# Performance work log

Hardware: AMD Instinct MI355X
Metric: run time of the kernel (lower is better)

Reference implementation:

```python
import jax, jax.numpy as jnp
import numpy as np
from math import sqrt

B, L, D, NH = 1, 2048, 1024, 16
HD = D // NH
EPS = 1e-5
NEG = -1e9


def setup_inputs() -> dict:
    key = jax.random.key(0)
    ks = jax.random.split(key, 5)
    x = jax.random.normal(ks[0], (B, L, D), jnp.float32)
    # causal additive mask (added to raw QK^T scores before /sqrt(d))
    causal = jnp.tril(jnp.ones((L, L), bool))
    m = jnp.where(causal, 0.0, NEG).astype(jnp.float32)[None, None]  # (1,1,L,L)
    init = lambda k, s: (0.02 * jax.random.normal(k, s)).astype(jnp.float32)
    return dict(
        x=x, m=m,
        wx_w=init(ks[1], (3 * D, D)), wx_b=jnp.zeros((3 * D,), jnp.float32),
        wo_w=init(ks[2], (D, D)), wo_b=jnp.zeros((D,), jnp.float32),
        ffn1_w=init(ks[3], (4 * D, D)), ffn1_b=jnp.zeros((4 * D,), jnp.float32),
        ffn2_w=init(ks[4], (D, 4 * D)), ffn2_b=jnp.zeros((D,), jnp.float32),
        ln1_w=jnp.float32(1.0), ln1_b=jnp.float32(0.0),
        ln2_w=jnp.float32(1.0), ln2_b=jnp.float32(0.0),
    )


def layer_norm(x, w, b):
    # scalar gain/bias, biased variance via E[x^2] - E[x]^2 (as in source)
    mu = x.mean(-1, keepdims=True)
    mu2 = (x * x).mean(-1, keepdims=True)
    sigma = jnp.sqrt(mu2 - mu * mu + EPS)
    return w * (x - mu) / sigma + b


def gelu(x):
    return x * 0.5 * (1 + jax.scipy.special.erf(x / sqrt(2.0)))


def reference(x, m, wx_w, wx_b, wo_w, wo_b, ffn1_w, ffn1_b, ffn2_w, ffn2_b,
              ln1_w, ln1_b, ln2_w, ln2_b):
    b, l, d = x.shape
    qkv = layer_norm(x, ln1_w, ln1_b) @ wx_w.T + wx_b          # (b,l,3d)
    q, k, v = [t.reshape(b, l, NH, HD) for t in jnp.split(qkv, 3, axis=-1)]
    # mask added BEFORE scaling by 1/sqrt(d) -- faithful to source
    scores = (jnp.einsum('bind,bjnd->bnij', q, k) + m) / sqrt(d)  # (b,nh,l,l)
    A = jax.nn.softmax(scores, axis=-1)
    mha = jnp.einsum('bnij,bjnd->bind', A, v).reshape(b, l, d)
    x = x + mha @ wo_w.T + wo_b
    h = layer_norm(x, ln2_w, ln2_b)
    return x + gelu(h @ ffn1_w.T + ffn1_b) @ ffn2_w.T + ffn2_b
```

## Files before the change

kernel.cpp:

```cpp
#include <hip/hip_runtime.h>

typedef short bf16x8 __attribute__((ext_vector_type(8)));
typedef float f32x4 __attribute__((ext_vector_type(4)));
typedef unsigned short u16;

__device__ __forceinline__ u16 f2b(float f) {
  unsigned u = __builtin_bit_cast(unsigned, f);
  u += 0x7fffu + ((u >> 16) & 1u);
  return (u16)(u >> 16);
}
__device__ __forceinline__ float b2f(u16 h) {
  unsigned u = ((unsigned)h) << 16;
  return __builtin_bit_cast(float, u);
}

__device__ __forceinline__ void gload16(const void* g, void* l) {
  __builtin_amdgcn_global_load_lds(
      (const __attribute__((address_space(1))) unsigned*)g,
      (__attribute__((address_space(3))) unsigned*)l, 16, 0, 0);
}

__global__ __launch_bounds__(256) void prep_kernel(
    const float* __restrict__ s0, int n0, const float* __restrict__ s1, int n1,
    const float* __restrict__ s2, int n2, const float* __restrict__ s3, int n3,
    u16* __restrict__ d0, u16* __restrict__ d1, u16* __restrict__ d2, u16* __restrict__ d3,
    const float* __restrict__ x, u16* __restrict__ lnout,
    const float* __restrict__ wp, const float* __restrict__ bp) {
  __shared__ float red[8];
  if (blockIdx.x < 1024) {
    long long total = ((long long)n0 + n1 + n2 + n3) >> 2;
    long long stride = 1024LL * 256;
    for (long long i = (long long)blockIdx.x * 256 + threadIdx.x; i < total; i += stride) {
      long long e = i << 2;
      const float* sp; u16* dp; long long off;
      if (e < n0)                { sp = s0; dp = d0; off = e; }
      else if (e < n0 + n1)      { sp = s1; dp = d1; off = e - n0; }
      else if (e < n0 + n1 + n2) { sp = s2; dp = d2; off = e - n0 - n1; }
      else                       { sp = s3; dp = d3; off = e - n0 - n1 - n2; }
      float4 v = *(const float4*)(sp + off);
      ushort4 o;
      o.x = f2b(v.x); o.y = f2b(v.y); o.z = f2b(v.z); o.w = f2b(v.w);
      *(ushort4*)(dp + off) = o;
    }
    return;
  }
  int row = blockIdx.x - 1024;
  const float* xr = x + (size_t)row * 1024;
  float4 v = ((const float4*)xr)[threadIdx.x];
  float lsum = v.x + v.y + v.z + v.w;
  float lsq = v.x * v.x + v.y * v.y + v.z * v.z + v.w * v.w;
#pragma unroll
  for (int off = 32; off; off >>= 1) {
    lsum += __shfl_down(lsum, off);
    lsq += __shfl_down(lsq, off);
  }
  int wv_ = threadIdx.x >> 6, ln_ = threadIdx.x & 63;
  if (ln_ == 0) { red[wv_] = lsum; red[4 + wv_] = lsq; }
  __syncthreads();
  if (threadIdx.x == 0) {
    float ts = red[0] + red[1] + red[2] + red[3];
    float ts2 = red[4] + red[5] + red[6] + red[7];
    red[0] = ts; red[4] = ts2;
  }
  __syncthreads();
  float mu = red[0] * (1.0f / 1024.0f);
  float mu2 = red[4] * (1.0f / 1024.0f);
  float inv = 1.0f / sqrtf(mu2 - mu * mu + 1e-5f);
  float gw = *wp, gb = *bp;
  ushort4 o;
  o.x = f2b(gw * (v.x - mu) * inv + gb);
  o.y = f2b(gw * (v.y - mu) * inv + gb);
  o.z = f2b(gw * (v.z - mu) * inv + gb);
  o.w = f2b(gw * (v.w - mu) * inv + gb);
  ((ushort4*)lnout)[(size_t)row * 256 + threadIdx.x] = o;
}

__global__ __launch_bounds__(256) void reduce2(
    const float* __restrict__ p, const float* __restrict__ bias,
    const float* __restrict__ resid, float* __restrict__ out) {
  int i = blockIdx.x * 256 + threadIdx.x;
  float4 a = ((const float4*)p)[i];
  float4 b = ((const float4*)p)[i + 524288];
  float4 r = ((const float4*)resid)[i];
  float4 bb = ((const float4*)bias)[i & 255];
  float4 o;
  o.x = a.x + b.x + r.x + bb.x;
  o.y = a.y + b.y + r.y + bb.y;
  o.z = a.z + b.z + r.z + bb.z;
  o.w = a.w + b.w + r.w + bb.w;
  ((float4*)out)[i] = o;
}

__global__ __launch_bounds__(256) void reduce_ln(
    const float* __restrict__ p, const float* __restrict__ bias,
    const float* __restrict__ resid, float* __restrict__ x1out,
    u16* __restrict__ lnout,
    const float* __restrict__ wp, const float* __restrict__ bp) {
  int row = blockIdx.x;
  int i = row * 256 + threadIdx.x;
  float4 a = ((const float4*)p)[i];
  float4 b = ((const float4*)p)[i + 524288];
  float4 r = ((const float4*)resid)[i];
  float4 bb = ((const float4*)bias)[threadIdx.x];
  float4 v;
  v.x = a.x + b.x + r.x + bb.x;
  v.y = a.y + b.y + r.y + bb.y;
  v.z = a.z + b.z + r.z + bb.z;
  v.w = a.w + b.w + r.w + bb.w;
  ((float4*)x1out)[i] = v;
  float lsum = v.x + v.y + v.z + v.w;
  float lsq = v.x * v.x + v.y * v.y + v.z * v.z + v.w * v.w;
#pragma unroll
  for (int off = 32; off; off >>= 1) {
    lsum += __shfl_down(lsum, off);
    lsq += __shfl_down(lsq, off);
  }
  __shared__ float red[8];
  int wv_ = threadIdx.x >> 6, ln_ = threadIdx.x & 63;
  if (ln_ == 0) { red[wv_] = lsum; red[4 + wv_] = lsq; }
  __syncthreads();
  if (threadIdx.x == 0) {
    float ts = red[0] + red[1] + red[2] + red[3];
    float ts2 = red[4] + red[5] + red[6] + red[7];
    red[0] = ts; red[4] = ts2;
  }
  __syncthreads();
  float mu = red[0] * (1.0f / 1024.0f);
  float mu2 = red[4] * (1.0f / 1024.0f);
  float inv = 1.0f / sqrtf(mu2 - mu * mu + 1e-5f);
  float gw = *wp, gb = *bp;
  ushort4 o;
  o.x = f2b(gw * (v.x - mu) * inv + gb);
  o.y = f2b(gw * (v.y - mu) * inv + gb);
  o.z = f2b(gw * (v.z - mu) * inv + gb);
  o.w = f2b(gw * (v.w - mu) * inv + gb);
  ((ushort4*)lnout)[i] = o;
}

#define BN 128
#define BMT 64
#define BK 64

template <int EPI, bool SPLITX>
__global__ __launch_bounds__(256, 3) void gemm_bt(
    const u16* __restrict__ A, const u16* __restrict__ W,
    const float* __restrict__ bias, const float* __restrict__ resid,
    void* __restrict__ Cout, u16* __restrict__ vtout, int M, int N, int K) {
  constexpr int MR = BMT / 32;
  __shared__ __align__(16) u16 sA[2][BMT * BK];
  __shared__ __align__(16) u16 sB[2][BN * BK];
  const int tid = threadIdx.x;

  const int gx = gridDim.x, gy = gridDim.y;
  int bx, by;
  {
    int oxy = blockIdx.y * gx + blockIdx.x;
    int xcd = oxy & 7, pos = oxy >> 3;
    if (SPLITX) {
      int bxp = gx >> 3;
      bx = xcd * bxp + pos % bxp;
      by = pos / bxp;
    } else {
      int byp = gy >> 3;
      by = xcd * byp + pos % byp;
      bx = pos / byp;
    }
  }

  const int l = tid & 63;
  const int w = tid >> 6;
  const int wm = w >> 1, wn = w & 1;
  const int lr = l & 15, lg = l >> 4;

  f32x4 acc[MR][4] = {};

  const int r_st = tid >> 3;
  const int s_st = tid & 7;

  const u16* Abase = A + (size_t)(by * BMT) * K;
  const u16* Wbase = W + (size_t)(bx * BN) * K;
  const int NK = K / (BK * (int)gridDim.z);
  const int ktbase = (int)blockIdx.z * NK;

  auto stage = [&](int buf, int kt) {
    const int k0 = (ktbase + kt) * BK;
#pragma unroll
    for (int i = 0; i < BMT / 32; i++) {
      int r = i * 32 + r_st;
      int ss = s_st ^ (r & 7);
      gload16(Abase + (size_t)r * K + k0 + ss * 8, &sA[buf][(i * 256 + tid) * 8]);
    }
#pragma unroll
    for (int i = 0; i < 4; i++) {
      int r = i * 32 + r_st;
      int ss = s_st ^ (r & 7);
      gload16(Wbase + (size_t)r * K + k0 + ss * 8, &sB[buf][(i * 256 + tid) * 8]);
    }
  };

  auto compute = [&](int buf) {
#pragma unroll
    for (int kk = 0; kk < 2; kk++) {
      bf16x8 a[MR], b[4];
#pragma unroll
      for (int mr = 0; mr < MR; mr++) {
        int row = wm * (BMT / 2) + mr * 16 + lr;
        int ss = (kk * 4 + lg) ^ (row & 7);
        a[mr] = *(const bf16x8*)&sA[buf][row * 64 + ss * 8];
      }
#pragma unroll
      for (int nr = 0; nr < 4; nr++) {
        int row = wn * 64 + nr * 16 + lr;
        int ss = (kk * 4 + lg) ^ (row & 7);
        b[nr] = *(const bf16x8*)&sB[buf][row * 64 + ss * 8];
      }
#pragma unroll
      for (int mr = 0; mr < MR; mr++)
#pragma unroll
        for (int nr = 0; nr < 4; nr++)
          acc[mr][nr] = __builtin_amdgcn_mfma_f32_16x16x32_bf16(a[mr], b[nr], acc[mr][nr], 0, 0, 0);
    }
  };

  stage(0, 0);
  asm volatile("s_waitcnt vmcnt(0)" ::: "memory");
  __syncthreads();
  for (int kt = 0; kt < NK; kt++) {
    if (kt + 1 < NK) stage((kt + 1) & 1, kt + 1);
    compute(kt & 1);
    asm volatile("s_waitcnt vmcnt(0)" ::: "memory");
    __syncthreads();
  }

  const int crow0 = by * BMT + wm * (BMT / 2);
  const int ccol0 = bx * BN + wn * 64;

  if (EPI == 4) {
    float* P4 = (float*)Cout + (size_t)blockIdx.z * (size_t)M * N;
#pragma unroll
    for (int nr = 0; nr < 4; nr++) {
      int col = ccol0 + nr * 16 + lr;
#pragma unroll
      for (int mr = 0; mr < MR; mr++) {
        int rowb = crow0 + mr * 16 + lg * 4;
#pragma unroll
        for (int r = 0; r < 4; r++)
          P4[(size_t)(rowb + r) * N + col] = acc[mr][nr][r];
      }
    }
    return;
  }

  if (EPI == 3 && ccol0 >= 2048) {
    const int hd0 = ccol0 - 2048;
#pragma unroll
    for (int nr = 0; nr < 4; nr++) {
      int hd = hd0 + nr * 16 + lr;
      float bv = bias[ccol0 + nr * 16 + lr];
#pragma unroll
      for (int mr = 0; mr < MR; mr++) {
        int m0 = crow0 + mr * 16 + lg * 4;
        ushort4 o;
        o.x = f2b(acc[mr][nr][0] + bv);
        o.y = f2b(acc[mr][nr][1] + bv);
        o.z = f2b(acc[mr][nr][2] + bv);
        o.w = f2b(acc[mr][nr][3] + bv);
        *(ushort4*)&vtout[(size_t)hd * 2048 + m0] = o;
      }
    }
    return;
  }

#pragma unroll
  for (int nr = 0; nr < 4; nr++) {
    int col = ccol0 + nr * 16 + lr;
    float bv = bias[col];
#pragma unroll
    for (int mr = 0; mr < MR; mr++) {
      int rowb = crow0 + mr * 16 + lg * 4;
#pragma unroll
      for (int r = 0; r < 4; r++) {
        float v = acc[mr][nr][r] + bv;
        size_t off = (size_t)(rowb + r) * N + col;
        if (EPI == 2) {
          float u = 0.7978845608f * (v + 0.044715f * v * v * v);
          u = fminf(15.0f, fmaxf(-15.0f, u));
          float e = __expf(2.0f * u);
          float g = 0.5f * v * (1.0f + (e - 1.0f) / (e + 1.0f));
          ((u16*)Cout)[off] = f2b(g);
        } else {
          ((u16*)Cout)[off] = f2b(v);
        }
      }
    }
  }
}

__global__ __launch_bounds__(256) void attn_kernel(
    const u16* __restrict__ qkv, const u16* __restrict__ vt,
    float* __restrict__ O0, float* __restrict__ O1, float* __restrict__ O2v,
    float* __restrict__ l0p, float* __restrict__ l1p, float* __restrict__ l2p) {
  const int i = (int)blockIdx.x;
  int qb, sec, nsec;
  if (i < 24)      { qb = 31 - i / 3;        sec = i % 3;        nsec = 3; }
  else if (i < 48) { qb = 23 - (i - 24) / 2; sec = (i - 24) & 1; nsec = 2; }
  else             { qb = 59 - i;            sec = 0;            nsec = 1; }
  const int nt = qb + 1;
  const int t0 = (nt * sec) / nsec;
  const int t1 = (nt * (sec + 1)) / nsec;

  const int h = blockIdx.y;
  __shared__ __align__(16) u16 sK[2][64 * 64];
  __shared__ __align__(16) u16 sV[2][64 * 64];
  __shared__ __align__(16) u16 P[4][16 * 72];
  const int tid = threadIdx.x;
  const int l = tid & 63, w = tid >> 6;
  const int lr = l & 15, lg = l >> 4;
  const int qrow0 = qb * 64 + w * 16;
  const u16* kbase = qkv + 1024 + h * 64;
  const u16* vbase = vt + (size_t)(h * 64) * 2048;

  const int r_st = tid >> 3;
  const int s_st = tid & 7;

  auto stage = [&](int buf, int t) {
    const int j0 = t * 64;
#pragma unroll
    for (int i2 = 0; i2 < 2; i2++) {
      int r = i2 * 32 + r_st;
      int ss = s_st ^ (r & 7);
      gload16(kbase + (size_t)(j0 + r) * 3072 + ss * 8, &sK[buf][(i2 * 256 + tid) * 8]);
    }
#pragma unroll
    for (int i2 = 0; i2 < 2; i2++) {
      int r = i2 * 32 + r_st;
      int ss = s_st ^ (r & 7);
      gload16(vbase + (size_t)r * 2048 + j0 + ss * 8, &sV[buf][(i2 * 256 + tid) * 8]);
    }
  };

  bf16x8 aq[2];
#pragma unroll
  for (int kk = 0; kk < 2; kk++)
    aq[kk] = *(const bf16x8*)&qkv[(size_t)(qrow0 + lr) * 3072 + h * 64 + kk * 32 + lg * 8];

  f32x4 oa[4];
  float l_r[4] = {0.f, 0.f, 0.f, 0.f};
#pragma unroll
  for (int d = 0; d < 4; d++) oa[d] = f32x4{0.f, 0.f, 0.f, 0.f};

  auto compute = [&](int buf, int t, bool masked) {
    const int j0 = t * 64;
    f32x4 s[4] = {};
#pragma unroll
    for (int kk = 0; kk < 2; kk++) {
#pragma unroll
      for (int c = 0; c < 4; c++) {
        int row = c * 16 + lr;
        int ss = (kk * 4 + lg) ^ (row & 7);
        bf16x8 kf = *(const bf16x8*)&sK[buf][row * 64 + ss * 8];
        s[c] = __builtin_amdgcn_mfma_f32_16x16x32_bf16(aq[kk], kf, s[c], 0, 0, 0);
      }
    }

#pragma unroll
    for (int r = 0; r < 4; r++) {
      const int q = qrow0 + lg * 4 + r;
      float rs = 0.f;
#pragma unroll
      for (int c = 0; c < 4; c++) {
        float p = __expf(s[c][r] * 0.03125f);
        if (masked) {
          int j = j0 + c * 16 + lr;
          p = (j > q) ? 0.f : p;
        }
        u16 pb = f2b(p);
        P[w][(lg * 4 + r) * 72 + c * 16 + lr] = pb;
        rs += b2f(pb);
      }
      l_r[r] += rs;
    }

#pragma unroll
    for (int kk = 0; kk < 2; kk++) {
      bf16x8 pa = *(const bf16x8*)&P[w][lr * 72 + kk * 32 + lg * 8];
#pragma unroll
      for (int d = 0; d < 4; d++) {
        int row = d * 16 + lr;
        int ss = (kk * 4 + lg) ^ (row & 7);
        bf16x8 bv = *(const bf16x8*)&sV[buf][row * 64 + ss * 8];
        oa[d] = __builtin_amdgcn_mfma_f32_16x16x32_bf16(pa, bv, oa[d], 0, 0, 0);
      }
    }
  };

  const int ntile = t1 - t0;
  stage(0, t0);
  asm volatile("s_waitcnt vmcnt(0)" ::: "memory");
  __syncthreads();
  for (int ti = 0; ti < ntile; ti++) {
    const int t = t0 + ti;
    if (ti + 1 < ntile) stage((ti + 1) & 1, t + 1);
    compute(ti & 1, t, t == nt - 1);
    asm volatile("s_waitcnt vmcnt(0)" ::: "memory");
    __syncthreads();
  }

  float* Op = (sec == 0) ? O0 : (sec == 1) ? O1 : O2v;
  float* lp = (sec == 0) ? l0p : (sec == 1) ? l1p : l2p;
#pragma unroll
  for (int r = 0; r < 4; r++) {
#pragma unroll
    for (int off = 1; off < 16; off <<= 1) l_r[r] += __shfl_xor(l_r[r], off);
    int q = qrow0 + lg * 4 + r;
    if (lr == 0) lp[q * 16 + h] = l_r[r];
#pragma unroll
    for (int d = 0; d < 4; d++)
      Op[(size_t)q * 1024 + h * 64 + d * 16 + lr] = oa[d][r];
  }
}

__global__ __launch_bounds__(256) void attn_combine(
    const float* __restrict__ O0, const float* __restrict__ O1,
    const float* __restrict__ O2v,
    const float* __restrict__ l0p, const float* __restrict__ l1p,
    const float* __restrict__ l2p, u16* __restrict__ mhab) {
  const int row = blockIdx.x;
  const int t = threadIdx.x;
  const int h = t >> 4;
  float4 v = ((const float4*)(O0 + (size_t)row * 1024))[t];
  float ls = l0p[row * 16 + h];
  if (row >= 768) {
    float4 v1 = ((const float4*)(O1 + (size_t)row * 1024))[t];
    v.x += v1.x; v.y += v1.y; v.z += v1.z; v.w += v1.w;
    ls += l1p[row * 16 + h];
  }
  if (row >= 1536) {
    float4 v2 = ((const float4*)(O2v + (size_t)row * 1024))[t];
    v.x += v2.x; v.y += v2.y; v.z += v2.z; v.w += v2.w;
    ls += l2p[row * 16 + h];
  }
  float inv = 1.0f / ls;
  ushort4 o;
  o.x = f2b(v.x * inv); o.y = f2b(v.y * inv);
  o.z = f2b(v.z * inv); o.w = f2b(v.w * inv);
  ((ushort4*)(mhab + (size_t)row * 1024))[t] = o;
}

extern "C" void kernel_launch(void* const* d_in, const int* in_sizes, int n_in,
                              void* d_out, int out_size, void* d_ws, size_t ws_size,
                              hipStream_t stream) {
  const float* x    = (const float*)d_in[0];
  const float* wx_w = (const float*)d_in[2];
  const float* wx_b = (const float*)d_in[3];
  const float* wo_w = (const float*)d_in[4];
  const float* wo_b = (const float*)d_in[5];
  const float* f1_w = (const float*)d_in[6];
  const float* f1_b = (const float*)d_in[7];
  const float* f2_w = (const float*)d_in[8];
  const float* f2_b = (const float*)d_in[9];
  const float* ln1w = (const float*)d_in[10];
  const float* ln1b = (const float*)d_in[11];
  const float* ln2w = (const float*)d_in[12];
  const float* ln2b = (const float*)d_in[13];

  char* ws = (char*)d_ws;
  u16*   ln_x  = (u16*)(ws + 0);
  float* l0p   = (float*)(ws + 0);
  float* l1p   = (float*)(ws + 131072);
  float* l2p   = (float*)(ws + 262144);
  u16*   qkv   = (u16*)(ws + 4194304);
  float* part  = (float*)(ws + 0);
  u16*   mhab  = (u16*)(ws + 16777216);
  float* x1    = (float*)(ws + 20971520);
  float* O0    = (float*)(ws + 20971520);
  u16*   hbuf  = (u16*)(ws + 29360128);
  u16*   vt    = (u16*)(ws + 33554432);
  u16*   f1o   = (u16*)(ws + 33554432);
  float* O1    = (float*)(ws + 37748736);
  float* O2v   = (float*)(ws + 46137344) - (size_t)1536 * 1024;
  u16*   wxb16 = (u16*)(ws + 50331648);
  u16*   wob16 = (u16*)(ws + 56623104);
  u16*   f1b16 = (u16*)(ws + 58720256);
  u16*   f2b16 = (u16*)(ws + 67108864);

  prep_kernel<<<3072, 256, 0, stream>>>(wx_w, 3145728, wo_w, 1048576, f1_w, 4194304, f2_w, 4194304,
                                        wxb16, wob16, f1b16, f2b16, x, ln_x, ln1w, ln1b);
  gemm_bt<3, true><<<dim3(24, 32), 256, 0, stream>>>(ln_x, wxb16, wx_b, nullptr, qkv, vt, 2048, 3072, 1024);
  attn_kernel<<<dim3(60, 16), 256, 0, stream>>>(qkv, vt, O0, O1, O2v, l0p, l1p, l2p);
  attn_combine<<<2048, 256, 0, stream>>>(O0, O1, O2v, l0p, l1p, l2p, mhab);
  gemm_bt<4, false><<<dim3(8, 32, 2), 256, 0, stream>>>(mhab, wob16, wo_b, nullptr, part, nullptr, 2048, 1024, 1024);
  reduce_ln<<<2048, 256, 0, stream>>>(part, wo_b, x, x1, hbuf, ln2w, ln2b);
  gemm_bt<2, true><<<dim3(32, 32), 256, 0, stream>>>(hbuf, f1b16, f1_b, nullptr, f1o, nullptr, 2048, 4096, 1024);
  gemm_bt<4, false><<<dim3(8, 32, 2), 256, 0, stream>>>(f1o, f2b16, f2_b, nullptr, part, nullptr, 2048, 1024, 4096);
  reduce2<<<2048, 256, 0, stream>>>(part, f2_b, x1, (float*)d_out);
}
```

Before: 157.2 us.

## Overlap remaining weight bf16 conversion with the QKV GEMM via extra blocks

The prep kernel now converts only the QKV projection weights to bf16. Conversion of the output-projection and FFN weights moves into extra blocks appended to the QKV GEMM grid (24 -> 32 columns), so it runs alongside the GEMM tiles instead of ahead of them. The GEMM gains a logical grid width parameter so tile swizzling ignores the extra blocks. This shortens the critical path before the first GEMM, at the cost of the conversion blocks competing with GEMM tiles for bandwidth and CU slots.

```diff
diff --git a/kernel.cpp b/kernel.cpp
--- a/kernel.cpp
+++ b/kernel.cpp
@@ -21,26 +21,19 @@
 }
 
 __global__ __launch_bounds__(256) void prep_kernel(
-    const float* __restrict__ s0, int n0, const float* __restrict__ s1, int n1,
-    const float* __restrict__ s2, int n2, const float* __restrict__ s3, int n3,
-    u16* __restrict__ d0, u16* __restrict__ d1, u16* __restrict__ d2, u16* __restrict__ d3,
+    const float* __restrict__ wxsrc, int nwx, u16* __restrict__ wxdst,
     const float* __restrict__ x, u16* __restrict__ lnout,
     const float* __restrict__ wp, const float* __restrict__ bp) {
   __shared__ float red[8];
   if (blockIdx.x < 1024) {
-    long long total = ((long long)n0 + n1 + n2 + n3) >> 2;
+    long long total = (long long)nwx >> 2;
     long long stride = 1024LL * 256;
     for (long long i = (long long)blockIdx.x * 256 + threadIdx.x; i < total; i += stride) {
-      long long e = i << 2;
-      const float* sp; u16* dp; long long off;
-      if (e < n0)                { sp = s0; dp = d0; off = e; }
-      else if (e < n0 + n1)      { sp = s1; dp = d1; off = e - n0; }
-      else if (e < n0 + n1 + n2) { sp = s2; dp = d2; off = e - n0 - n1; }
-      else                       { sp = s3; dp = d3; off = e - n0 - n1 - n2; }
-      float4 v = *(const float4*)(sp + off);
+      long long off = i << 2;
+      float4 v = *(const float4*)(wxsrc + off);
       ushort4 o;
       o.x = f2b(v.x); o.y = f2b(v.y); o.z = f2b(v.z); o.w = f2b(v.w);
-      *(ushort4*)(dp + off) = o;
+      *(ushort4*)(wxdst + off) = o;
     }
     return;
   }
@@ -145,19 +138,43 @@
 __global__ __launch_bounds__(256, 3) void gemm_bt(
     const u16* __restrict__ A, const u16* __restrict__ W,
     const float* __restrict__ bias, const float* __restrict__ resid,
-    void* __restrict__ Cout, u16* __restrict__ vtout, int M, int N, int K) {
+    void* __restrict__ Cout, u16* __restrict__ vtout, int M, int N, int K,
+    int gxl,
+    const float* c0, int cn0, u16* cd0,
+    const float* c1, int cn1, u16* cd1,
+    const float* c2, int cn2, u16* cd2) {
   constexpr int MR = BMT / 32;
   __shared__ __align__(16) u16 sA[2][BMT * BK];
   __shared__ __align__(16) u16 sB[2][BN * BK];
   const int tid = threadIdx.x;
 
-  const int gx = gridDim.x, gy = gridDim.y;
+  const int gy = gridDim.y;
+  const int nblk = gxl * gy;
+  const int lin = (int)blockIdx.y * (int)gridDim.x + (int)blockIdx.x;
+
+  if (lin >= nblk) {
+    long long total = ((long long)cn0 + cn1 + cn2) >> 2;
+    long long stride = (long long)((int)gridDim.x * gy - nblk) * 256;
+    for (long long i = (long long)(lin - nblk) * 256 + tid; i < total; i += stride) {
+      long long e = i << 2;
+      const float* sp; u16* dp; long long off;
+      if (e < cn0)            { sp = c0; dp = cd0; off = e; }
+      else if (e < cn0 + cn1) { sp = c1; dp = cd1; off = e - cn0; }
+      else                    { sp = c2; dp = cd2; off = e - cn0 - cn1; }
+      float4 v = *(const float4*)(sp + off);
+      ushort4 o;
+      o.x = f2b(v.x); o.y = f2b(v.y); o.z = f2b(v.z); o.w = f2b(v.w);
+      *(ushort4*)(dp + off) = o;
+    }
+    return;
+  }
+
   int bx, by;
   {
-    int oxy = blockIdx.y * gx + blockIdx.x;
+    int oxy = lin;
     int xcd = oxy & 7, pos = oxy >> 3;
     if (SPLITX) {
-      int bxp = gx >> 3;
+      int bxp = gxl >> 3;
       bx = xcd * bxp + pos % bxp;
       by = pos / bxp;
     } else {
@@ -484,14 +501,21 @@
   u16*   f1b16 = (u16*)(ws + 58720256);
   u16*   f2b16 = (u16*)(ws + 67108864);
 
-  prep_kernel<<<3072, 256, 0, stream>>>(wx_w, 3145728, wo_w, 1048576, f1_w, 4194304, f2_w, 4194304,
-                                        wxb16, wob16, f1b16, f2b16, x, ln_x, ln1w, ln1b);
-  gemm_bt<3, true><<<dim3(24, 32), 256, 0, stream>>>(ln_x, wxb16, wx_b, nullptr, qkv, vt, 2048, 3072, 1024);
+  prep_kernel<<<3072, 256, 0, stream>>>(wx_w, 3145728, wxb16, x, ln_x, ln1w, ln1b);
+  gemm_bt<3, true><<<dim3(32, 32), 256, 0, stream>>>(
+      ln_x, wxb16, wx_b, nullptr, qkv, vt, 2048, 3072, 1024, 24,
+      wo_w, 1048576, wob16, f1_w, 4194304, f1b16, f2_w, 4194304, f2b16);
   attn_kernel<<<dim3(60, 16), 256, 0, stream>>>(qkv, vt, O0, O1, O2v, l0p, l1p, l2p);
   attn_combine<<<2048, 256, 0, stream>>>(O0, O1, O2v, l0p, l1p, l2p, mhab);
-  gemm_bt<4, false><<<dim3(8, 32, 2), 256, 0, stream>>>(mhab, wob16, wo_b, nullptr, part, nullptr, 2048, 1024, 1024);
+  gemm_bt<4, false><<<dim3(8, 32, 2), 256, 0, stream>>>(
+      mhab, wob16, wo_b, nullptr, part, nullptr, 2048, 1024, 1024, 8,
+      nullptr, 0, nullptr, nullptr, 0, nullptr, nullptr, 0, nullptr);
   reduce_ln<<<2048, 256, 0, stream>>>(part, wo_b, x, x1, hbuf, ln2w, ln2b);
-  gemm_bt<2, true><<<dim3(32, 32), 256, 0, stream>>>(hbuf, f1b16, f1_b, nullptr, f1o, nullptr, 2048, 4096, 1024);
-  gemm_bt<4, false><<<dim3(8, 32, 2), 256, 0, stream>>>(f1o, f2b16, f2_b, nullptr, part, nullptr, 2048, 1024, 4096);
+  gemm_bt<2, true><<<dim3(32, 32), 256, 0, stream>>>(
+      hbuf, f1b16, f1_b, nullptr, f1o, nullptr, 2048, 4096, 1024, 32,
+      nullptr, 0, nullptr, nullptr, 0, nullptr, nullptr, 0, nullptr);
+  gemm_bt<4, false><<<dim3(8, 32, 2), 256, 0, stream>>>(
+      f1o, f2b16, f2_b, nullptr, part, nullptr, 2048, 1024, 4096, 8,
+      nullptr, 0, nullptr, nullptr, 0, nullptr, nullptr, 0, nullptr);
   reduce2<<<2048, 256, 0, stream>>>(part, f2_b, x1, (float*)d_out);
 }
```

Measured after the change: 162.7 us. +3.5%, slower.
